# Kernel tuning notes

Hardware: AMD Instinct MI355X
Metric: run time of the kernel (lower is better)

## Reference

```python
import jax, jax.numpy as jnp
import numpy as np

N_NODES = 50000
N_EDGES = 800000
IN_FEATS = 256
HIDDEN = 128
HEADS = 2
NEG_SLOPE = 0.2


def gat_conv(x, edge_index, W, att_src, att_dst, bias, heads, out_c, concat):
    """PyG-style GATConv: linear -> per-edge attention logits -> segment
    softmax over destination neighborhoods -> scatter-add aggregate.
    Self-loops are added (PyG default add_self_loops=True)."""
    N = x.shape[0]
    h = (x @ W.T).reshape(N, heads, out_c)           # [N,H,C]
    loop = jnp.arange(N)
    src = jnp.concatenate([edge_index[0], loop])      # [E+N]
    dst = jnp.concatenate([edge_index[1], loop])
    a_src = jnp.sum(h * att_src, axis=-1)             # [N,H]
    a_dst = jnp.sum(h * att_dst, axis=-1)
    alpha = a_src[src] + a_dst[dst]                   # [E+N,H]
    alpha = jax.nn.leaky_relu(alpha, NEG_SLOPE)
    amax = jax.ops.segment_max(alpha, dst, num_segments=N)
    alpha = jnp.exp(alpha - amax[dst])
    denom = jax.ops.segment_sum(alpha, dst, num_segments=N)
    alpha = alpha / denom[dst]
    msg = h[src] * alpha[..., None]                   # [E+N,H,C]
    out = jax.ops.segment_sum(msg, dst, num_segments=N)  # [N,H,C]
    if concat:
        out = out.reshape(N, heads * out_c)
    else:
        out = out.mean(axis=1)
    return out + bias


def setup_inputs() -> dict:
    key = jax.random.key(0)
    ks = jax.random.split(key, 12)
    x = jax.random.normal(ks[0], (N_NODES, IN_FEATS), dtype=jnp.float32)
    edge_index = jax.random.randint(ks[1], (2, N_EDGES), 0, N_NODES, dtype=jnp.int64)
    s = 0.1
    W1 = jax.random.normal(ks[2], (HEADS * HIDDEN, IN_FEATS), dtype=jnp.float32) * s
    att_src1 = jax.random.normal(ks[3], (1, HEADS, HIDDEN), dtype=jnp.float32) * s
    att_dst1 = jax.random.normal(ks[4], (1, HEADS, HIDDEN), dtype=jnp.float32) * s
    b1 = jnp.zeros((HEADS * HIDDEN,), dtype=jnp.float32)
    W2 = jax.random.normal(ks[5], (HIDDEN, HEADS * HIDDEN), dtype=jnp.float32) * s
    att_src2 = jax.random.normal(ks[6], (1, 1, HIDDEN), dtype=jnp.float32) * s
    att_dst2 = jax.random.normal(ks[7], (1, 1, HIDDEN), dtype=jnp.float32) * s
    b2 = jnp.zeros((HIDDEN,), dtype=jnp.float32)
    return {"x": x, "edge_index": edge_index,
            "W1": W1, "att_src1": att_src1, "att_dst1": att_dst1, "b1": b1,
            "W2": W2, "att_src2": att_src2, "att_dst2": att_dst2, "b2": b2}


def reference(x, edge_index, W1, att_src1, att_dst1, b1, W2, att_src2, att_dst2, b2):
    h = gat_conv(x, edge_index, W1, att_src1, att_dst1, b1, HEADS, HIDDEN, True)
    h = jax.nn.relu(h)
    out = gat_conv(h, edge_index, W2, att_src2, att_dst2, b2, 1, HIDDEN, False)
    return out
```

## Files before the change

kernel.cpp:

```cpp
#include <hip/hip_runtime.h>
#include <hip/hip_bf16.h>


typedef _Float16 half8v __attribute__((ext_vector_type(8)));
typedef _Float16 half4v __attribute__((ext_vector_type(4)));
typedef _Float16 half2v __attribute__((ext_vector_type(2)));
typedef float f32x4 __attribute__((ext_vector_type(4)));


template <typename TA, int H>
__global__ __launch_bounds__(256) void gemm_att_kernel(
    const TA* __restrict__ A,
    const float* __restrict__ B,
    _Float16* __restrict__ C,
    const float* __restrict__ att_s,
    const float* __restrict__ att_d,
    float* __restrict__ a_s,
    float* __restrict__ a_d,
    int M, int K)
{
    constexpr int BM = 128, BK = 32, LDA = 40;
    constexpr int NCOL = H * 128;
    __shared__ _Float16 Ah[BM * LDA];
    __shared__ _Float16 Bh[BM * LDA];
    __shared__ float red[2][2][64][2];

    const int tid = threadIdx.x;
    const int m0 = blockIdx.x * BM;
    const int by = blockIdx.y;
    const int n0 = by * 128;
    const int w  = tid >> 6;
    const int l  = tid & 63;
    const int wm = (w >> 1) * 64;
    const int wn = (w & 1) * 64;
    const int lr = l & 15;
    const int lq = l >> 4;

    f32x4 acc[4][4] = {};

    for (int k0 = 0; k0 < K; k0 += BK) {
        if constexpr (__is_same(TA, float)) {
#pragma unroll
            for (int it = 0; it < 4; ++it) {
                const int row = (tid >> 3) + it * 32;
                const int gm  = min(m0 + row, M - 1);
                const int c4  = (tid & 7) * 4;
                float4 v = *reinterpret_cast<const float4*>(A + (long)gm * K + k0 + c4);
                half4v o = { (_Float16)v.x, (_Float16)v.y, (_Float16)v.z, (_Float16)v.w };
                *reinterpret_cast<half4v*>(&Ah[row * LDA + c4]) = o;
            }
        } else {
#pragma unroll
            for (int it = 0; it < 2; ++it) {
                const int row = (tid >> 2) + it * 64;
                const int gm  = min(m0 + row, M - 1);
                const int c8  = (tid & 3) * 8;
                float4 v = *reinterpret_cast<const float4*>((const char*)A + ((long)gm * K + k0 + c8) * 2);
                *reinterpret_cast<float4*>(&Ah[row * LDA + c8]) = v;
            }
        }
#pragma unroll
        for (int it = 0; it < 4; ++it) {
            const int row = (tid >> 3) + it * 32;
            const int c4  = (tid & 7) * 4;
            float4 v = *reinterpret_cast<const float4*>(B + (long)(n0 + row) * K + k0 + c4);
            half4v o = { (_Float16)v.x, (_Float16)v.y, (_Float16)v.z, (_Float16)v.w };
            *reinterpret_cast<half4v*>(&Bh[row * LDA + c4]) = o;
        }
        __syncthreads();

        half8v af[4], bf[4];
#pragma unroll
        for (int i = 0; i < 4; ++i)
            af[i] = *reinterpret_cast<const half8v*>(&Ah[(wm + i * 16 + lr) * LDA + lq * 8]);
#pragma unroll
        for (int j = 0; j < 4; ++j)
            bf[j] = *reinterpret_cast<const half8v*>(&Bh[(wn + j * 16 + lr) * LDA + lq * 8]);
#pragma unroll
        for (int i = 0; i < 4; ++i)
#pragma unroll
            for (int j = 0; j < 4; ++j)
                acc[i][j] = __builtin_amdgcn_mfma_f32_16x16x32_f16(af[i], bf[j], acc[i][j], 0, 0, 0);
        __syncthreads();
    }

#pragma unroll
    for (int i = 0; i < 4; ++i) {
        const int gm_base = m0 + wm + i * 16 + lq * 4;
#pragma unroll
        for (int r = 0; r < 4; ++r) {
            const int gm = gm_base + r;
            if (gm < M) {
#pragma unroll
                for (int j = 0; j < 4; ++j)
                    C[(long)gm * NCOL + n0 + wn + j * 16 + lr] = (_Float16)acc[i][j][r];
            }
        }
    }

    float asv[4], adv[4];
#pragma unroll
    for (int j = 0; j < 4; ++j) {
        asv[j] = att_s[n0 + wn + j * 16 + lr];
        adv[j] = att_d[n0 + wn + j * 16 + lr];
    }
    float ps[4][4] = {}, pd[4][4] = {};
#pragma unroll
    for (int i = 0; i < 4; ++i)
#pragma unroll
        for (int j = 0; j < 4; ++j)
#pragma unroll
            for (int r = 0; r < 4; ++r) {
                ps[i][r] += acc[i][j][r] * asv[j];
                pd[i][r] += acc[i][j][r] * adv[j];
            }
#pragma unroll
    for (int o = 1; o < 16; o <<= 1)
#pragma unroll
        for (int i = 0; i < 4; ++i)
#pragma unroll
            for (int r = 0; r < 4; ++r) {
                ps[i][r] += __shfl_xor(ps[i][r], o, 64);
                pd[i][r] += __shfl_xor(pd[i][r], o, 64);
            }
    if (lr == 0) {
#pragma unroll
        for (int i = 0; i < 4; ++i)
#pragma unroll
            for (int r = 0; r < 4; ++r) {
                const int row = i * 16 + lq * 4 + r;
                red[wm >> 6][wn >> 6][row][0] = ps[i][r];
                red[wm >> 6][wn >> 6][row][1] = pd[i][r];
            }
    }
    __syncthreads();
    if (wn == 0) {
        const int row = l;
        const int gm = m0 + wm + row;
        if (gm < M) {
            const int wi = wm >> 6;
            a_s[(long)gm * H + by] = red[wi][0][row][0] + red[wi][1][row][0];
            a_d[(long)gm * H + by] = red[wi][0][row][1] + red[wi][1][row][1];
        }
    }
}


__global__ void count_kernel(const int* __restrict__ dst, int* __restrict__ deg, int E)
{
    const int tid = blockIdx.x * blockDim.x + threadIdx.x;
    const int e4 = tid * 4;
    if (e4 + 3 < E) {
        const int4 d = *reinterpret_cast<const int4*>(dst + e4);
        atomicAdd(&deg[d.x], 1);
        atomicAdd(&deg[d.y], 1);
        atomicAdd(&deg[d.z], 1);
        atomicAdd(&deg[d.w], 1);
    } else if (e4 < E) {
        for (int k = e4; k < E; ++k) atomicAdd(&deg[dst[k]], 1);
    }
}

__global__ __launch_bounds__(256) void block_scan_kernel(
    const int* __restrict__ deg, int* __restrict__ pre, int* __restrict__ blk, int n)
{
    __shared__ int s[256];
    const int t = threadIdx.x;
    const int base = blockIdx.x * 1024 + t * 4;
    int4 d = make_int4(-1, -1, -1, -1);
    if (base + 3 < n) d = *reinterpret_cast<const int4*>(deg + base);
    else {
        if (base + 0 < n) d.x = deg[base + 0];
        if (base + 1 < n) d.y = deg[base + 1];
        if (base + 2 < n) d.z = deg[base + 2];
        if (base + 3 < n) d.w = deg[base + 3];
    }
    const int v0 = d.x + 1, v1 = d.y + 1, v2 = d.z + 1, v3 = d.w + 1;
    s[t] = v0 + v1 + v2 + v3;
    __syncthreads();
#pragma unroll
    for (int o = 1; o < 256; o <<= 1) {
        int val = 0;
        if (t >= o) val = s[t - o];
        __syncthreads();
        s[t] += val;
        __syncthreads();
    }
    int run = (t == 0) ? 0 : s[t - 1];
    int4 o4;
    o4.x = run; run += v0;
    o4.y = run; run += v1;
    o4.z = run; run += v2;
    o4.w = run; run += v3;
    if (base + 3 < n) *reinterpret_cast<int4*>(pre + base) = o4;
    else {
        if (base + 0 < n) pre[base + 0] = o4.x;
        if (base + 1 < n) pre[base + 1] = o4.y;
        if (base + 2 < n) pre[base + 2] = o4.z;
        if (base + 3 < n) pre[base + 3] = o4.w;
    }
    if (t == 255) blk[blockIdx.x] = s[255];
}

__global__ __launch_bounds__(256) void finalize_scan_kernel(
    const int* __restrict__ pre, const int* __restrict__ blk,
    int* __restrict__ off, int* __restrict__ cursor, int n, int nvb)
{
    __shared__ int s_add;
    const int vb = blockIdx.x;
    const int t  = threadIdx.x;
    if (t < 64) {
        int v = (t < vb) ? blk[t] : 0;
#pragma unroll
        for (int o = 32; o > 0; o >>= 1) v += __shfl_xor(v, o, 64);
        if (t == 0) s_add = v;
    }
    __syncthreads();
    const int add = s_add;
    const int base = vb * 1024 + t * 4;
    if (base + 3 < n) {
        int4 p = *reinterpret_cast<const int4*>(pre + base);
        p.x += add; p.y += add; p.z += add; p.w += add;
        *reinterpret_cast<int4*>(off + base) = p;
        *reinterpret_cast<int4*>(cursor + base) = p;
    } else {
#pragma unroll
        for (int k = 0; k < 4; ++k)
            if (base + k < n) {
                const int v = pre[base + k] + add;
                off[base + k] = v;
                cursor[base + k] = v;
            }
    }
    if (vb == nvb - 1 && t == 0) off[n] = add + blk[vb];
}

__global__ void scatter_kernel(const int* __restrict__ src, const int* __restrict__ dst,
                               int* __restrict__ cursor, int* __restrict__ csr_src,
                               int E, int N)
{
    const int tid = blockIdx.x * blockDim.x + threadIdx.x;
    const int nq = (E + 3) / 4;
    if (tid < nq) {
        const int e4 = tid * 4;
        if (e4 + 3 < E) {
            const int4 sv = *reinterpret_cast<const int4*>(src + e4);
            const int4 dv = *reinterpret_cast<const int4*>(dst + e4);
            csr_src[atomicAdd(&cursor[dv.x], 1)] = sv.x;
            csr_src[atomicAdd(&cursor[dv.y], 1)] = sv.y;
            csr_src[atomicAdd(&cursor[dv.z], 1)] = sv.z;
            csr_src[atomicAdd(&cursor[dv.w], 1)] = sv.w;
        } else {
            for (int k = e4; k < E; ++k)
                csr_src[atomicAdd(&cursor[dst[k]], 1)] = src[k];
        }
    } else {
        const int nn = tid - nq;
        if (nn < N) csr_src[atomicAdd(&cursor[nn], 1)] = nn;
    }
}


#define AGG_TILE 64

template <int H, int C, int VPT, bool RELU, typename TOUT>
__global__ __launch_bounds__(H * C / VPT) void aggregate_kernel(
    const int* __restrict__ csr_off,
    const int* __restrict__ csr_src,
    const _Float16* __restrict__ h,
    const float* __restrict__ a_s,
    const float* __restrict__ a_d,
    const float* __restrict__ bias,
    TOUT* __restrict__ out)
{
    const int d   = blockIdx.x;
    const int t   = threadIdx.x;
    const int col = t * VPT;
    const int hh  = col / C;

    __shared__ int   s_src[AGG_TILE];
    __shared__ float s_w[AGG_TILE][H];

    const int beg = csr_off[d];
    const int end = csr_off[d + 1];

    float acc[VPT] = {};
    float wsum = 0.f;

    for (int base = beg; base < end; base += AGG_TILE) {
        const int len = min(AGG_TILE, end - base);
        if (t < len) {
            const int s = csr_src[base + t];
            s_src[t] = s;
#pragma unroll
            for (int h2 = 0; h2 < H; ++h2) {
                float logit = a_s[s * H + h2] + a_d[d * H + h2];
                logit = logit > 0.f ? logit : 0.2f * logit;
                s_w[t][h2] = __expf(logit);
            }
        }
        __syncthreads();
#pragma unroll 4
        for (int j = 0; j < len; ++j) {
            const float w = s_w[j][hh];
            const int   s = s_src[j];
            if constexpr (VPT == 4) {
                half4v hv = *reinterpret_cast<const half4v*>(h + (long)s * (H * C) + col);
                acc[0] += w * (float)hv.x;
                acc[1] += w * (float)hv.y;
                acc[2] += w * (float)hv.z;
                acc[3] += w * (float)hv.w;
            } else {
                half2v hv = *reinterpret_cast<const half2v*>(h + (long)s * (H * C) + col);
                acc[0] += w * (float)hv.x;
                acc[1] += w * (float)hv.y;
            }
            wsum += w;
        }
        __syncthreads();
    }

    const float inv = 1.f / wsum;
    float r[VPT];
#pragma unroll
    for (int k = 0; k < VPT; ++k) {
        r[k] = acc[k] * inv + bias[col + k];
        if (RELU) r[k] = r[k] > 0.f ? r[k] : 0.f;
    }
    if constexpr (__is_same(TOUT, _Float16)) {
#pragma unroll
        for (int k = 0; k < VPT; ++k)
            out[(long)d * (H * C) + col + k] = (_Float16)r[k];
    } else {
#pragma unroll
        for (int k = 0; k < VPT; ++k)
            out[(long)d * (H * C) + col + k] = r[k];
    }
}


extern "C" void kernel_launch(void* const* d_in, const int* in_sizes, int n_in,
                              void* d_out, int out_size, void* d_ws, size_t ws_size,
                              hipStream_t stream)
{
    const float* x    = (const float*)d_in[0];
    const int*   eidx = (const int*)d_in[1];
    const float* W1   = (const float*)d_in[2];
    const float* as1  = (const float*)d_in[3];
    const float* ad1  = (const float*)d_in[4];
    const float* b1   = (const float*)d_in[5];
    const float* W2   = (const float*)d_in[6];
    const float* as2  = (const float*)d_in[7];
    const float* ad2  = (const float*)d_in[8];
    const float* b2   = (const float*)d_in[9];
    float* out = (float*)d_out;

    const int IN_FEATS = 256;
    const int N = in_sizes[0] / IN_FEATS;
    const int E = in_sizes[1] / 2;

    const int* esrc = eidx;
    const int* edst = eidx + E;

    size_t off = 0;
    auto alloc = [&](size_t bytes) -> void* {
        void* p = (char*)d_ws + off;
        off += (bytes + 255) & ~(size_t)255;
        return p;
    };
    _Float16* h1h   = (_Float16*)alloc((size_t)N * 256 * 2);
    _Float16* o1h   = (_Float16*)alloc((size_t)N * 256 * 2);
    _Float16* h2h   = (_Float16*)alloc((size_t)N * 128 * 2);
    float* a1s      = (float*)alloc((size_t)N * 2 * 4);
    float* a1d      = (float*)alloc((size_t)N * 2 * 4);
    float* a2s      = (float*)alloc((size_t)N * 4);
    float* a2d      = (float*)alloc((size_t)N * 4);
    int*   deg      = (int*)alloc((size_t)N * 4);
    int*   pre      = (int*)alloc((size_t)N * 4);
    int*   cursor   = (int*)alloc((size_t)N * 4);
    int*   csr_off  = (int*)alloc((size_t)(N + 1) * 4);
    int*   csr_src  = (int*)alloc((size_t)(E + N) * 4);
    int*   blk      = (int*)alloc(64 * 4);

    const int nvb = (N + 1023) / 1024;

    hipMemsetAsync(deg, 0, (size_t)N * 4, stream);
    count_kernel<<<((E + 3) / 4 + 255) / 256, 256, 0, stream>>>(edst, deg, E);
    block_scan_kernel<<<nvb, 256, 0, stream>>>(deg, pre, blk, N);
    finalize_scan_kernel<<<nvb, 256, 0, stream>>>(pre, blk, csr_off, cursor, N, nvb);
    {
        const int nThr = (E + 3) / 4 + N;
        scatter_kernel<<<(nThr + 255) / 256, 256, 0, stream>>>(
            esrc, edst, cursor, csr_src, E, N);
    }

    {
        dim3 grid((N + 127) / 128, 2);
        gemm_att_kernel<float, 2><<<grid, 256, 0, stream>>>(
            x, W1, h1h, as1, ad1, a1s, a1d, N, 256);
    }
    aggregate_kernel<2, 128, 4, true, _Float16><<<N, 64, 0, stream>>>(
        csr_off, csr_src, h1h, a1s, a1d, b1, o1h);

    {
        dim3 grid((N + 127) / 128, 1);
        gemm_att_kernel<_Float16, 1><<<grid, 256, 0, stream>>>(
            o1h, W2, h2h, as2, ad2, a2s, a2d, N, 256);
    }
    aggregate_kernel<1, 128, 2, false, float><<<N, 64, 0, stream>>>(
        csr_off, csr_src, h2h, a2s, a2d, b2, out);
}
```

Before: 337.9 us.

## Fold CSR edge scatter into first GEMM and self-loops into scan finalize

Removes the standalone scatter kernel. Self-loop entries are now written directly by the scan-finalize kernel at the first slot of each destination segment, with the cursor starting one past it. The edge scatter loop runs as a grid-stride prologue inside the layer-1 GEMM kernel, saving a launch and letting the atomic scatter share the GPU with GEMM work. In exchange, the GEMM blocks are delayed by the scatter prologue, and the order of neighbours within each segment changes.

```diff
diff --git a/kernel.cpp b/kernel.cpp
--- a/kernel.cpp
+++ b/kernel.cpp
@@ -8,7 +8,7 @@
 typedef float f32x4 __attribute__((ext_vector_type(4)));
 
 
-template <typename TA, int H>
+template <typename TA, int H, bool SCATTER>
 __global__ __launch_bounds__(256) void gemm_att_kernel(
     const TA* __restrict__ A,
     const float* __restrict__ B,
@@ -17,7 +17,9 @@
     const float* __restrict__ att_d,
     float* __restrict__ a_s,
     float* __restrict__ a_d,
-    int M, int K)
+    int M, int K,
+    const int* __restrict__ esrc, const int* __restrict__ edst,
+    int* __restrict__ cursor, int* __restrict__ csr_src, int E)
 {
     constexpr int BM = 128, BK = 32, LDA = 40;
     constexpr int NCOL = H * 128;
@@ -26,6 +28,27 @@
     __shared__ float red[2][2][64][2];
 
     const int tid = threadIdx.x;
+
+    if constexpr (SCATTER) {
+        const int nq   = (E + 3) >> 2;
+        const int nblk = gridDim.x * gridDim.y;
+        const int bid  = blockIdx.y * gridDim.x + blockIdx.x;
+        for (int q = bid * 256 + tid; q < nq; q += nblk * 256) {
+            const int e4 = q * 4;
+            if (e4 + 3 < E) {
+                const int4 sv = *reinterpret_cast<const int4*>(esrc + e4);
+                const int4 dv = *reinterpret_cast<const int4*>(edst + e4);
+                csr_src[atomicAdd(&cursor[dv.x], 1)] = sv.x;
+                csr_src[atomicAdd(&cursor[dv.y], 1)] = sv.y;
+                csr_src[atomicAdd(&cursor[dv.z], 1)] = sv.z;
+                csr_src[atomicAdd(&cursor[dv.w], 1)] = sv.w;
+            } else {
+                for (int k = e4; k < E; ++k)
+                    csr_src[atomicAdd(&cursor[edst[k]], 1)] = esrc[k];
+            }
+        }
+    }
+
     const int m0 = blockIdx.x * BM;
     const int by = blockIdx.y;
     const int n0 = by * 128;
@@ -204,7 +227,8 @@
 
 __global__ __launch_bounds__(256) void finalize_scan_kernel(
     const int* __restrict__ pre, const int* __restrict__ blk,
-    int* __restrict__ off, int* __restrict__ cursor, int n, int nvb)
+    int* __restrict__ off, int* __restrict__ cursor, int* __restrict__ csr_src,
+    int n, int nvb)
 {
     __shared__ int s_add;
     const int vb = blockIdx.x;
@@ -222,42 +246,23 @@
         int4 p = *reinterpret_cast<const int4*>(pre + base);
         p.x += add; p.y += add; p.z += add; p.w += add;
         *reinterpret_cast<int4*>(off + base) = p;
-        *reinterpret_cast<int4*>(cursor + base) = p;
+        int4 c = make_int4(p.x + 1, p.y + 1, p.z + 1, p.w + 1);
+        *reinterpret_cast<int4*>(cursor + base) = c;
+        csr_src[p.x] = base + 0;
+        csr_src[p.y] = base + 1;
+        csr_src[p.z] = base + 2;
+        csr_src[p.w] = base + 3;
     } else {
 #pragma unroll
         for (int k = 0; k < 4; ++k)
             if (base + k < n) {
                 const int v = pre[base + k] + add;
                 off[base + k] = v;
-                cursor[base + k] = v;
+                cursor[base + k] = v + 1;
+                csr_src[v] = base + k;
             }
     }
     if (vb == nvb - 1 && t == 0) off[n] = add + blk[vb];
-}
-
-__global__ void scatter_kernel(const int* __restrict__ src, const int* __restrict__ dst,
-                               int* __restrict__ cursor, int* __restrict__ csr_src,
-                               int E, int N)
-{
-    const int tid = blockIdx.x * blockDim.x + threadIdx.x;
-    const int nq = (E + 3) / 4;
-    if (tid < nq) {
-        const int e4 = tid * 4;
-        if (e4 + 3 < E) {
-            const int4 sv = *reinterpret_cast<const int4*>(src + e4);
-            const int4 dv = *reinterpret_cast<const int4*>(dst + e4);
-            csr_src[atomicAdd(&cursor[dv.x], 1)] = sv.x;
-            csr_src[atomicAdd(&cursor[dv.y], 1)] = sv.y;
-            csr_src[atomicAdd(&cursor[dv.z], 1)] = sv.z;
-            csr_src[atomicAdd(&cursor[dv.w], 1)] = sv.w;
-        } else {
-            for (int k = e4; k < E; ++k)
-                csr_src[atomicAdd(&cursor[dst[k]], 1)] = src[k];
-        }
-    } else {
-        const int nn = tid - nq;
-        if (nn < N) csr_src[atomicAdd(&cursor[nn], 1)] = nn;
-    }
 }
 
 
@@ -387,25 +392,22 @@
     hipMemsetAsync(deg, 0, (size_t)N * 4, stream);
     count_kernel<<<((E + 3) / 4 + 255) / 256, 256, 0, stream>>>(edst, deg, E);
     block_scan_kernel<<<nvb, 256, 0, stream>>>(deg, pre, blk, N);
-    finalize_scan_kernel<<<nvb, 256, 0, stream>>>(pre, blk, csr_off, cursor, N, nvb);
-    {
-        const int nThr = (E + 3) / 4 + N;
-        scatter_kernel<<<(nThr + 255) / 256, 256, 0, stream>>>(
-            esrc, edst, cursor, csr_src, E, N);
-    }
+    finalize_scan_kernel<<<nvb, 256, 0, stream>>>(pre, blk, csr_off, cursor, csr_src, N, nvb);
 
     {
         dim3 grid((N + 127) / 128, 2);
-        gemm_att_kernel<float, 2><<<grid, 256, 0, stream>>>(
-            x, W1, h1h, as1, ad1, a1s, a1d, N, 256);
+        gemm_att_kernel<float, 2, true><<<grid, 256, 0, stream>>>(
+            x, W1, h1h, as1, ad1, a1s, a1d, N, 256,
+            esrc, edst, cursor, csr_src, E);
     }
     aggregate_kernel<2, 128, 4, true, _Float16><<<N, 64, 0, stream>>>(
         csr_off, csr_src, h1h, a1s, a1d, b1, o1h);
 
     {
         dim3 grid((N + 127) / 128, 1);
-        gemm_att_kernel<_Float16, 1><<<grid, 256, 0, stream>>>(
-            o1h, W2, h2h, as2, ad2, a2s, a2d, N, 256);
+        gemm_att_kernel<_Float16, 1, false><<<grid, 256, 0, stream>>>(
+            o1h, W2, h2h, as2, ad2, a2s, a2d, N, 256,
+            nullptr, nullptr, nullptr, nullptr, 0);
     }
     aggregate_kernel<1, 128, 2, false, float><<<N, 64, 0, stream>>>(
         csr_off, csr_src, h2h, a2s, a2d, b2, out);
```

Result: faster. 323.7 us (-4.2%).
